# Optimization experiments

Measured on AMD Instinct MI355X. Metric: run time of the kernel, lower is better.

Reference implementation:

```python
import jax, jax.numpy as jnp
import numpy as np

EPS = 1e-07

def ternary_quantize(w, gamma=1.0):
    # gamma' = gamma / (mean|W| + eps)
    w_bar = jnp.mean(jnp.abs(w))
    gamma_prime = gamma / (w_bar + EPS)
    q = jnp.where(w > 0.5, 1.0, jnp.where(w < -0.5, -1.0, 0.0)).astype(w.dtype)
    # RoundClip(gamma' * q, -1, 1); jnp.round matches torch.round (half-to-even)
    return jnp.clip(jnp.round(gamma_prime * q), -1.0, 1.0)

def setup_inputs() -> dict:
    key = jax.random.key(0)
    kx, kw = jax.random.split(key)
    x = jax.random.normal(kx, (4, 2048, 4096), dtype=jnp.float32)
    weight = jax.random.normal(kw, (4096, 4096), dtype=jnp.float32)  # [out, in]
    return {"x": x, "weight": weight}

def reference(x, weight):
    wq = ternary_quantize(weight)
    # F.linear: x @ W^T
    return jnp.einsum('bsi,oi->bso', x, wq)
```

## Files before the change

### kernel.cpp

```cpp
#include <hip/hip_runtime.h>
#include <hip/hip_bf16.h>
#include <stdint.h>


typedef __bf16 bf16x8 __attribute__((ext_vector_type(8)));
typedef float  f32x4  __attribute__((ext_vector_type(4)));

#define EPS 1e-7f
#define NPART 4096

__device__ __forceinline__ void async_load16(const void* g, void* l) {
    __builtin_amdgcn_global_load_lds(
        (__attribute__((address_space(1))) void*)(const_cast<void*>(g)),
        (__attribute__((address_space(3))) void*)l,
        16, 0, 0);
}

__device__ __forceinline__ unsigned short f2bf_rne(float f) {
    unsigned u = __float_as_uint(f);
    unsigned r = (u + 0x7fffu + ((u >> 16) & 1u)) >> 16;
    return (unsigned short)r;
}

__device__ __forceinline__ float scale_from_partials(const float* __restrict__ partials,
                                                     float invCount) {
    const int lane = threadIdx.x & 63;
    const float4* p4 = (const float4*)partials;
    float s = 0.0f;
    #pragma unroll
    for (int j = 0; j < NPART / 4 / 64; ++j) {
        float4 v = p4[lane + 64 * j];
        s += v.x + v.y + v.z + v.w;
    }
    #pragma unroll
    for (int off = 32; off > 0; off >>= 1) s += __shfl_down(s, off, 64);
    s = __shfl(s, 0, 64);
    float mean = s * invCount;
    float gp = 1.0f / (mean + EPS);
    return fminf(fmaxf(rintf(gp), -1.0f), 1.0f);
}


__device__ __forceinline__ unsigned short tern_bf16(float w) {
    return (w > 0.5f) ? (unsigned short)0x3F80u
         : ((w < -0.5f) ? (unsigned short)0xBF80u : (unsigned short)0u);
}

__global__ __launch_bounds__(256) void quant_w_bf16(
    const float* __restrict__ in, ushort4* __restrict__ out,
    float* __restrict__ partials, int n4)
{
    int tid = blockIdx.x * blockDim.x + threadIdx.x;
    int stride = gridDim.x * blockDim.x;
    float s = 0.0f;
    for (int i = tid; i < n4; i += stride) {
        float4 v = ((const float4*)in)[i];
        s += fabsf(v.x) + fabsf(v.y) + fabsf(v.z) + fabsf(v.w);
        ushort4 r;
        r.x = tern_bf16(v.x); r.y = tern_bf16(v.y);
        r.z = tern_bf16(v.z); r.w = tern_bf16(v.w);
        out[i] = r;
    }
    #pragma unroll
    for (int off = 32; off > 0; off >>= 1) s += __shfl_down(s, off, 64);
    __shared__ float psum[4];
    int lane = threadIdx.x & 63, wid = threadIdx.x >> 6;
    if (lane == 0) psum[wid] = s;
    __syncthreads();
    if (threadIdx.x == 0)
        partials[blockIdx.x] = psum[0] + psum[1] + psum[2] + psum[3];
}


__global__ __launch_bounds__(256) void conv_x_bf16(
    const float* __restrict__ in, ushort4* __restrict__ out, int n4)
{
    int i = blockIdx.x * blockDim.x + threadIdx.x;
    if (i < n4) {
        float4 v = ((const float4*)in)[i];
        ushort4 r;
        r.x = f2bf_rne(v.x); r.y = f2bf_rne(v.y);
        r.z = f2bf_rne(v.z); r.w = f2bf_rne(v.w);
        out[i] = r;
    }
}


#define BM 256
#define BN 256
#define BK 32

#define GEMM_TILE(t_, CUR, NXT)                                                \
  {                                                                            \
    const int tA = ((t_) + 1 < T) ? ((t_) + 1) : (t_);                         \
    const int tB = ((t_) + 2 < T) ? ((t_) + 2) : (t_);                         \
    bf16x8 a[8], b[4];                                                         \
    _Pragma("unroll")                                                          \
    for (int mt = 0; mt < 8; ++mt)                                             \
      a[mt] = *(const bf16x8*)&As[CUR][wr][(mt * 16 + lm) * BK + slot8];       \
    _Pragma("unroll")                                                          \
    for (int nt = 0; nt < 4; ++nt)                                             \
      b[nt] = *(const bf16x8*)&Bs[CUR][wh][(wb + nt * 16 + lm) * BK + slot8];  \
    async_load16(gA + (size_t)tA * BK,        &As[NXT][0][(size_t)tid * 8]);   \
    async_load16(gA + gH1 + (size_t)tA * BK,  &As[NXT][1][(size_t)tid * 8]);   \
    __builtin_amdgcn_s_barrier();                                              \
    asm volatile("s_waitcnt lgkmcnt(0)" ::: "memory");                         \
    __builtin_amdgcn_s_setprio(1);                                             \
    _Pragma("unroll")                                                          \
    for (int mt = 0; mt < 8; ++mt) {                                           \
      acc[mt][0] = __builtin_amdgcn_mfma_f32_16x16x32_bf16(a[mt], b[0], acc[mt][0], 0, 0, 0); \
      acc[mt][1] = __builtin_amdgcn_mfma_f32_16x16x32_bf16(a[mt], b[1], acc[mt][1], 0, 0, 0); \
    }                                                                          \
    __builtin_amdgcn_s_setprio(0);                                             \
    __builtin_amdgcn_s_barrier();                                              \
    async_load16(gB + (size_t)tB * BK,        &Bs[CUR][0][(size_t)tid * 8]);   \
    async_load16(gB + gH1 + (size_t)tB * BK,  &Bs[CUR][1][(size_t)tid * 8]);   \
    __builtin_amdgcn_s_barrier();                                              \
    __builtin_amdgcn_s_setprio(1);                                             \
    _Pragma("unroll")                                                          \
    for (int mt = 0; mt < 8; ++mt) {                                           \
      acc[mt][2] = __builtin_amdgcn_mfma_f32_16x16x32_bf16(a[mt], b[2], acc[mt][2], 0, 0, 0); \
      acc[mt][3] = __builtin_amdgcn_mfma_f32_16x16x32_bf16(a[mt], b[3], acc[mt][3], 0, 0, 0); \
    }                                                                          \
    __builtin_amdgcn_s_setprio(0);                                             \
    asm volatile("s_waitcnt vmcnt(2)" ::: "memory");                           \
    __builtin_amdgcn_s_barrier();                                              \
  }

__global__ __launch_bounds__(512, 2) void gemm_bt(
    const __bf16* __restrict__ A,
    const __bf16* __restrict__ B,
    float* __restrict__ C,
    const float* __restrict__ partials,
    int N, int K, float invCount)
{
    __shared__ __bf16 As[2][2][128 * BK];
    __shared__ __bf16 Bs[2][2][128 * BK];

    const int tid  = threadIdx.x;
    const int lane = tid & 63;
    const int wid  = tid >> 6;
    const int wr   = wid >> 2;
    const int wc   = wid & 3;
    const int wh   = wc >> 1;
    const int wb   = (wc & 1) * 64;
    const int lm   = lane & 15;
    const int quad = lane >> 4;

    const int gx  = gridDim.x;
    const int nwg = gx * gridDim.y;
    int wg = blockIdx.y * gx + blockIdx.x;
    wg = (wg & 7) * (nwg >> 3) + (wg >> 3);
    const int mBase = (wg / gx) * BM;
    const int nBase = (wg % gx) * BN;

    const int srow = tid >> 2;
    const int scc  = (tid & 3) ^ (srow & 3) ^ ((srow >> 2) & 3);
    const int slot8 = (quad ^ (lm & 3) ^ ((lm >> 2) & 3)) * 8;

    const __bf16* gA = A + (size_t)(mBase + srow) * K + scc * 8;
    const __bf16* gB = B + (size_t)(nBase + srow) * K + scc * 8;
    const size_t gH1 = (size_t)128 * K;

    const int T = K / BK;
    f32x4 acc[8][4] = {};

    {
        const size_t k1 = (T > 1) ? BK : 0;
        async_load16(gB,            &Bs[0][0][(size_t)tid * 8]);
        async_load16(gB + gH1,      &Bs[0][1][(size_t)tid * 8]);
        async_load16(gA,            &As[0][0][(size_t)tid * 8]);
        async_load16(gA + gH1,      &As[0][1][(size_t)tid * 8]);
        async_load16(gB + k1,       &Bs[1][0][(size_t)tid * 8]);
        async_load16(gB + gH1 + k1, &Bs[1][1][(size_t)tid * 8]);
    }
    asm volatile("s_waitcnt vmcnt(2)" ::: "memory");
    __builtin_amdgcn_s_barrier();

    for (int t = 0; t < T; t += 2) {
        GEMM_TILE(t,     0, 1);
        GEMM_TILE(t + 1, 1, 0);
    }
    asm volatile("s_waitcnt vmcnt(0)" ::: "memory");

    const float tscale = scale_from_partials(partials, invCount);

    #pragma unroll
    for (int mt = 0; mt < 8; ++mt) {
        #pragma unroll
        for (int nt = 0; nt < 4; ++nt) {
            #pragma unroll
            for (int r = 0; r < 4; ++r) {
                int row = mBase + wr * 128 + mt * 16 + quad * 4 + r;
                int col = nBase + wc * 64 + nt * 16 + lm;
                C[(size_t)row * N + col] = tscale * acc[mt][nt][r];
            }
        }
    }
}


__global__ void gemm_fallback(const float* __restrict__ x, const float* __restrict__ w,
                              float* __restrict__ out, const float* __restrict__ partials,
                              int N, int K, float invCount)
{
    __shared__ float xs[16][17];
    __shared__ float qs[16][17];
    int tx = threadIdx.x & 15;
    int ty = threadIdx.x >> 4;
    int row = blockIdx.y * 16 + ty;
    int col = blockIdx.x * 16 + tx;
    float acc = 0.0f;
    for (int k0 = 0; k0 < K; k0 += 16) {
        xs[ty][tx] = x[(size_t)row * K + k0 + tx];
        float wv = w[(size_t)(blockIdx.x * 16 + ty) * K + k0 + tx];
        qs[ty][tx] = (wv > 0.5f) ? 1.0f : ((wv < -0.5f) ? -1.0f : 0.0f);
        __syncthreads();
        #pragma unroll
        for (int j = 0; j < 16; ++j) acc += xs[ty][j] * qs[tx][j];
        __syncthreads();
    }
    float tscale = scale_from_partials(partials, invCount);
    out[(size_t)row * N + col] = tscale * acc;
}

__global__ __launch_bounds__(256) void absmean_only(
    const float* __restrict__ w, float* __restrict__ partials, int n4)
{
    int tid = blockIdx.x * blockDim.x + threadIdx.x;
    int stride = gridDim.x * blockDim.x;
    float s = 0.0f;
    for (int i = tid; i < n4; i += stride) {
        float4 v = ((const float4*)w)[i];
        s += fabsf(v.x) + fabsf(v.y) + fabsf(v.z) + fabsf(v.w);
    }
    #pragma unroll
    for (int off = 32; off > 0; off >>= 1) s += __shfl_down(s, off, 64);
    __shared__ float psum[4];
    int lane = threadIdx.x & 63, wid = threadIdx.x >> 6;
    if (lane == 0) psum[wid] = s;
    __syncthreads();
    if (threadIdx.x == 0)
        partials[blockIdx.x] = psum[0] + psum[1] + psum[2] + psum[3];
}


extern "C" void kernel_launch(void* const* d_in, const int* in_sizes, int n_in,
                              void* d_out, int out_size, void* d_ws, size_t ws_size,
                              hipStream_t stream) {
    const float* x = (const float*)d_in[0];
    const float* w = (const float*)d_in[1];
    float* out = (float*)d_out;

    const int K = 4096;
    const int M = in_sizes[0] / K;
    const int N = in_sizes[1] / K;
    const float invCount = 1.0f / (float)(in_sizes[1]);

    float* partials = (float*)d_ws;
    const size_t base = NPART * sizeof(float);
    const size_t need = base + (size_t)M * K * 2 + (size_t)N * K * 2;

    const bool shapes_ok = (M % BM == 0) && (N % BN == 0) && (K % (2 * BK) == 0);

    if (ws_size >= need && shapes_ok) {
        __bf16* xb = (__bf16*)((char*)d_ws + base);
        __bf16* qb = (__bf16*)((char*)d_ws + base + (size_t)M * K * 2);

        int xn4 = (M * K) / 4;
        int wn4 = (N * K) / 4;
        quant_w_bf16<<<NPART, 256, 0, stream>>>(w, (ushort4*)qb, partials, wn4);
        conv_x_bf16<<<(xn4 + 255) / 256, 256, 0, stream>>>(x, (ushort4*)xb, xn4);

        dim3 grid(N / BN, M / BM);
        gemm_bt<<<grid, 512, 0, stream>>>(xb, qb, out, partials, N, K, invCount);
    } else {
        absmean_only<<<NPART, 256, 0, stream>>>(w, partials, in_sizes[1] / 4);
        dim3 grid(N / 16, M / 16);
        gemm_fallback<<<grid, 256, 0, stream>>>(x, w, out, partials, N, K, invCount);
    }
}
```

Before: 524.3 us.

## Double BK to 64 with 128KB dynamic LDS and quadrant-interleaved MFMA pipeline

Raises the K tile from 32 to 64 and moves the GEMM's LDS buffers into 128KB of dynamic shared memory. The main loop is restructured into four quadrant MFMA phases, with async global-to-LDS stages spread between them and an 8-way XOR swizzle for the wider rows. The aim is fewer barriers per unit of K and better overlap of loads with MFMA work. The larger LDS footprint likely cuts occupancy from two workgroups per CU to one. The kernel also depends on the dynamic-LDS attribute succeeding, and falls back to the slow path if it does not.

```diff
diff --git a/kernel.cpp b/kernel.cpp
--- a/kernel.cpp
+++ b/kernel.cpp
@@ -88,42 +88,81 @@
 
 #define BM 256
 #define BN 256
-#define BK 32
-
-#define GEMM_TILE(t_, CUR, NXT)                                                \
+#define BK 64
+
+#define LDSA(buf, h) (ldsbuf + ((buf) * 2 + (h)) * 8192)
+#define LDSB(buf, h) (ldsbuf + 32768 + ((buf) * 2 + (h)) * 8192)
+
+#define STAGE(dst, p, tt, h)                                                   \
   {                                                                            \
-    const int tA = ((t_) + 1 < T) ? ((t_) + 1) : (t_);                         \
-    const int tB = ((t_) + 2 < T) ? ((t_) + 2) : (t_);                         \
-    bf16x8 a[8], b[4];                                                         \
+    __bf16* d_ = (dst);                                                        \
+    const __bf16* s_ = (p) + (size_t)(tt) * BK + (size_t)(h) * 128 * K;        \
+    async_load16(s_,                 d_ + (size_t)tid * 8);                    \
+    async_load16(s_ + (size_t)64 * K, d_ + 4096 + (size_t)tid * 8);            \
+  }
+
+#define READ_A(buf, qm)                                                        \
+  _Pragma("unroll")                                                            \
+  for (int i = 0; i < 4; ++i) {                                                \
+    const __bf16* r_ = LDSA(buf, wr) + ((qm) * 64 + i * 16 + lm) * 64;         \
+    areg[i][0] = *(const bf16x8*)(r_ + sl0);                                   \
+    areg[i][1] = *(const bf16x8*)(r_ + sl1);                                   \
+  }
+
+#define READ_B(buf, qn, dst)                                                   \
+  _Pragma("unroll")                                                            \
+  for (int j = 0; j < 2; ++j) {                                                \
+    const __bf16* r_ = LDSB(buf, wh) + (wb + (qn) * 32 + j * 16 + lm) * 64;    \
+    dst[j][0] = *(const bf16x8*)(r_ + sl0);                                    \
+    dst[j][1] = *(const bf16x8*)(r_ + sl1);                                    \
+  }
+
+#define MFMA16(qm, qn, breg)                                                   \
+  __builtin_amdgcn_s_setprio(1);                                               \
+  _Pragma("unroll")                                                            \
+  for (int i = 0; i < 4; ++i) {                                                \
     _Pragma("unroll")                                                          \
-    for (int mt = 0; mt < 8; ++mt)                                             \
-      a[mt] = *(const bf16x8*)&As[CUR][wr][(mt * 16 + lm) * BK + slot8];       \
-    _Pragma("unroll")                                                          \
-    for (int nt = 0; nt < 4; ++nt)                                             \
-      b[nt] = *(const bf16x8*)&Bs[CUR][wh][(wb + nt * 16 + lm) * BK + slot8];  \
-    async_load16(gA + (size_t)tA * BK,        &As[NXT][0][(size_t)tid * 8]);   \
-    async_load16(gA + gH1 + (size_t)tA * BK,  &As[NXT][1][(size_t)tid * 8]);   \
+    for (int j = 0; j < 2; ++j) {                                              \
+      acc[(qm) * 4 + i][(qn) * 2 + j] = __builtin_amdgcn_mfma_f32_16x16x32_bf16( \
+          areg[i][0], breg[j][0], acc[(qm) * 4 + i][(qn) * 2 + j], 0, 0, 0);   \
+      acc[(qm) * 4 + i][(qn) * 2 + j] = __builtin_amdgcn_mfma_f32_16x16x32_bf16( \
+          areg[i][1], breg[j][1], acc[(qm) * 4 + i][(qn) * 2 + j], 0, 0, 0);   \
+    }                                                                          \
+  }                                                                            \
+  __builtin_amdgcn_s_setprio(0);
+
+#define LGKM0                                                                  \
+  asm volatile("s_waitcnt lgkmcnt(0)" ::: "memory");                           \
+  __builtin_amdgcn_sched_barrier(0);
+
+#define TILE(tt, CUR, NXT)                                                     \
+  {                                                                            \
+    const int tA = ((tt) + 1 < T) ? ((tt) + 1) : (T - 1);                      \
+    const int tB = ((tt) + 2 < T) ? ((tt) + 2) : (T - 1);                      \
+    bf16x8 areg[4][2], b0[2][2], b1[2][2];                                     \
+                                                                       \
+    READ_A(CUR, 0);                                                            \
+    READ_B(CUR, 0, b0);                                                        \
+    STAGE(LDSA(NXT, 0), pA, tA, 0);                                            \
+    LGKM0;                                                                     \
+    MFMA16(0, 0, b0);                                                          \
     __builtin_amdgcn_s_barrier();                                              \
-    asm volatile("s_waitcnt lgkmcnt(0)" ::: "memory");                         \
-    __builtin_amdgcn_s_setprio(1);                                             \
-    _Pragma("unroll")                                                          \
-    for (int mt = 0; mt < 8; ++mt) {                                           \
-      acc[mt][0] = __builtin_amdgcn_mfma_f32_16x16x32_bf16(a[mt], b[0], acc[mt][0], 0, 0, 0); \
-      acc[mt][1] = __builtin_amdgcn_mfma_f32_16x16x32_bf16(a[mt], b[1], acc[mt][1], 0, 0, 0); \
-    }                                                                          \
-    __builtin_amdgcn_s_setprio(0);                                             \
+                                                                       \
+    READ_B(CUR, 1, b1);                                                        \
+    STAGE(LDSA(NXT, 1), pA, tA, 1);                                            \
+    LGKM0;                                                                     \
+    MFMA16(0, 1, b1);                                                          \
     __builtin_amdgcn_s_barrier();                                              \
-    async_load16(gB + (size_t)tB * BK,        &Bs[CUR][0][(size_t)tid * 8]);   \
-    async_load16(gB + gH1 + (size_t)tB * BK,  &Bs[CUR][1][(size_t)tid * 8]);   \
+                                                                       \
+    READ_A(CUR, 1);                                                            \
+    STAGE(LDSB(CUR, 0), pB, tB, 0);                                            \
+    LGKM0;                                                                     \
+    MFMA16(1, 1, b1);                                                          \
     __builtin_amdgcn_s_barrier();                                              \
-    __builtin_amdgcn_s_setprio(1);                                             \
-    _Pragma("unroll")                                                          \
-    for (int mt = 0; mt < 8; ++mt) {                                           \
-      acc[mt][2] = __builtin_amdgcn_mfma_f32_16x16x32_bf16(a[mt], b[2], acc[mt][2], 0, 0, 0); \
-      acc[mt][3] = __builtin_amdgcn_mfma_f32_16x16x32_bf16(a[mt], b[3], acc[mt][3], 0, 0, 0); \
-    }                                                                          \
-    __builtin_amdgcn_s_setprio(0);                                             \
-    asm volatile("s_waitcnt vmcnt(2)" ::: "memory");                           \
+                                                           \
+    STAGE(LDSB(CUR, 1), pB, tB, 1);                                            \
+    MFMA16(1, 0, b0);                                                          \
+    asm volatile("s_waitcnt vmcnt(4)" ::: "memory");                           \
     __builtin_amdgcn_s_barrier();                                              \
   }
 
@@ -134,8 +173,7 @@
     const float* __restrict__ partials,
     int N, int K, float invCount)
 {
-    __shared__ __bf16 As[2][2][128 * BK];
-    __shared__ __bf16 Bs[2][2][128 * BK];
+    extern __shared__ __bf16 ldsbuf[];
 
     const int tid  = threadIdx.x;
     const int lane = tid & 63;
@@ -147,6 +185,9 @@
     const int lm   = lane & 15;
     const int quad = lane >> 4;
 
+    const int sl0 = ((0 * 4 + quad) ^ (lm & 7)) * 8;
+    const int sl1 = ((1 * 4 + quad) ^ (lm & 7)) * 8;
+
     const int gx  = gridDim.x;
     const int nwg = gx * gridDim.y;
     int wg = blockIdx.y * gx + blockIdx.x;
@@ -154,34 +195,32 @@
     const int mBase = (wg / gx) * BM;
     const int nBase = (wg % gx) * BN;
 
-    const int srow = tid >> 2;
-    const int scc  = (tid & 3) ^ (srow & 3) ^ ((srow >> 2) & 3);
-    const int slot8 = (quad ^ (lm & 3) ^ ((lm >> 2) & 3)) * 8;
-
-    const __bf16* gA = A + (size_t)(mBase + srow) * K + scc * 8;
-    const __bf16* gB = B + (size_t)(nBase + srow) * K + scc * 8;
-    const size_t gH1 = (size_t)128 * K;
+    const int row0 = tid >> 3;
+    const int cc0  = (tid & 7) ^ (row0 & 7);
+    const __bf16* pA = A + (size_t)(mBase + row0) * K + cc0 * 8;
+    const __bf16* pB = B + (size_t)(nBase + row0) * K + cc0 * 8;
 
     const int T = K / BK;
     f32x4 acc[8][4] = {};
 
+    STAGE(LDSA(0, 0), pA, 0, 0);
+    STAGE(LDSA(0, 1), pA, 0, 1);
+    STAGE(LDSB(0, 0), pB, 0, 0);
+    STAGE(LDSB(0, 1), pB, 0, 1);
     {
-        const size_t k1 = (T > 1) ? BK : 0;
-        async_load16(gB,            &Bs[0][0][(size_t)tid * 8]);
-        async_load16(gB + gH1,      &Bs[0][1][(size_t)tid * 8]);
-        async_load16(gA,            &As[0][0][(size_t)tid * 8]);
-        async_load16(gA + gH1,      &As[0][1][(size_t)tid * 8]);
-        async_load16(gB + k1,       &Bs[1][0][(size_t)tid * 8]);
-        async_load16(gB + gH1 + k1, &Bs[1][1][(size_t)tid * 8]);
-    }
-    asm volatile("s_waitcnt vmcnt(2)" ::: "memory");
+        const int t1 = (T > 1) ? 1 : 0;
+        STAGE(LDSB(1, 0), pB, t1, 0);
+        STAGE(LDSB(1, 1), pB, t1, 1);
+    }
+    asm volatile("s_waitcnt vmcnt(4)" ::: "memory");
     __builtin_amdgcn_s_barrier();
 
     for (int t = 0; t < T; t += 2) {
-        GEMM_TILE(t,     0, 1);
-        GEMM_TILE(t + 1, 1, 0);
+        TILE(t,     0, 1);
+        TILE(t + 1, 1, 0);
     }
     asm volatile("s_waitcnt vmcnt(0)" ::: "memory");
+    __builtin_amdgcn_s_barrier();
 
     const float tscale = scale_from_partials(partials, invCount);
 
@@ -261,9 +300,17 @@
     const size_t base = NPART * sizeof(float);
     const size_t need = base + (size_t)M * K * 2 + (size_t)N * K * 2;
 
+    static int big_lds_ok = -1;
+    if (big_lds_ok < 0) {
+        hipError_t e = hipFuncSetAttribute((const void*)gemm_bt,
+                                           hipFuncAttributeMaxDynamicSharedMemorySize,
+                                           131072);
+        big_lds_ok = (e == hipSuccess) ? 1 : 0;
+    }
+
     const bool shapes_ok = (M % BM == 0) && (N % BN == 0) && (K % (2 * BK) == 0);
 
-    if (ws_size >= need && shapes_ok) {
+    if (ws_size >= need && shapes_ok && big_lds_ok == 1) {
         __bf16* xb = (__bf16*)((char*)d_ws + base);
         __bf16* qb = (__bf16*)((char*)d_ws + base + (size_t)M * K * 2);
 
@@ -273,7 +320,7 @@
         conv_x_bf16<<<(xn4 + 255) / 256, 256, 0, stream>>>(x, (ushort4*)xb, xn4);
 
         dim3 grid(N / BN, M / BM);
-        gemm_bt<<<grid, 512, 0, stream>>>(xb, qb, out, partials, N, K, invCount);
+        gemm_bt<<<grid, 512, 131072, stream>>>(xb, qb, out, partials, N, K, invCount);
     } else {
         absmean_only<<<NPART, 256, 0, stream>>>(w, partials, in_sizes[1] / 4);
         dim3 grid(N / 16, M / 16);
```

Result: faster. 459.0 us (-12.4%).
